# Kernel optimization log

Measured on AMD Instinct MI355X. Metric: run time of the kernel, lower is better.

## Reference

```python
import jax, jax.numpy as jnp
import numpy as np

B, L, D, H = 2, 2048, 1024, 16
HD = D // H


def setup_inputs() -> dict:
    key = jax.random.key(0)
    ks = jax.random.split(key, 14)
    s = 0.02
    return {
        "hidden_states": jax.random.normal(ks[0], (B, L, D), jnp.float32),
        "position_embeddings": jax.random.normal(ks[1], (B, L, D), jnp.float32),
        "Wcq": jax.random.normal(ks[2], (D, D), jnp.float32) * s,
        "bcq": jnp.zeros((D,), jnp.float32),
        "Wck": jax.random.normal(ks[3], (D, D), jnp.float32) * s,
        "bck": jnp.zeros((D,), jnp.float32),
        "Wpq": jax.random.normal(ks[4], (D, D), jnp.float32) * s,
        "bpq": jnp.zeros((D,), jnp.float32),
        "Wpk": jax.random.normal(ks[5], (D, D), jnp.float32) * s,
        "bpk": jnp.zeros((D,), jnp.float32),
        "rel_bias": jnp.zeros((1, H, 1, 1), jnp.float32),
        "Wo": jax.random.normal(ks[6], (D, D), jnp.float32) * s,
        "bo": jnp.zeros((D,), jnp.float32),
    }


def _split_heads(x):
    # [B, L, D] -> [B, H, L, HD]
    b, l, _ = x.shape
    return x.reshape(b, l, H, HD).transpose(0, 2, 1, 3)


def reference(hidden_states, position_embeddings, Wcq, bcq, Wck, bck,
              Wpq, bpq, Wpk, bpk, rel_bias, Wo, bo):
    cq = _split_heads(hidden_states @ Wcq + bcq)
    ck = _split_heads(hidden_states @ Wck + bck)
    # NOTE: original code (faithfully reproduced) uses content_key as the value
    cv = ck
    pq = _split_heads(position_embeddings @ Wpq + bpq)
    pk = _split_heads(position_embeddings @ Wpk + bpk)

    scores = (jnp.einsum("bhqd,bhkd->bhqk", cq, ck)
              + jnp.einsum("bhqd,bhkd->bhqk", pq, pk)
              + rel_bias)
    attn_weights = jax.nn.softmax(scores / jnp.sqrt(jnp.float32(HD)), axis=-1)
    ctx = jnp.einsum("bhqk,bhkd->bhqd", attn_weights, cv)
    ctx = ctx.transpose(0, 2, 1, 3).reshape(hidden_states.shape[0], -1, D)
    output = ctx @ Wo + bo
    return output, attn_weights
```

## Files before the change

kernel.cpp:

```cpp
#include <hip/hip_runtime.h>
#include <hip/hip_bf16.h>
#include <math.h>


#define Bc 2
#define Lc 2048
#define Dc 1024
#define Hc 16
#define Mc (Bc*Lc)
#define NT 32

typedef __attribute__((ext_vector_type(8))) __bf16 bf16x8;
typedef __attribute__((ext_vector_type(4))) float f32x4;
typedef __attribute__((ext_vector_type(16))) float f32x16;
typedef __attribute__((ext_vector_type(2))) unsigned u32x2;

union U4 { unsigned u[4]; bf16x8 v; };

__device__ __forceinline__ void gl_lds16(const void* g, void* l) {
    __builtin_amdgcn_global_load_lds(
        (const __attribute__((address_space(1))) void*)g,
        (__attribute__((address_space(3))) void*)l, 16, 0, 0);
}
__device__ __forceinline__ unsigned pkbf(float a, float b) {
    unsigned short ua = __builtin_bit_cast(unsigned short, (__bf16)a);
    unsigned short ub = __builtin_bit_cast(unsigned short, (__bf16)b);
    return (unsigned)ua | ((unsigned)ub << 16);
}
__device__ __forceinline__ float lo2f(unsigned u){ return __builtin_bit_cast(float, u << 16); }
__device__ __forceinline__ float hi2f(unsigned u){ return __builtin_bit_cast(float, u & 0xffff0000u); }
#define E2(x) __builtin_amdgcn_exp2f(x)

#define WAIT_VM0  asm volatile("s_waitcnt vmcnt(0)" ::: "memory")
#define WAIT_VM2  asm volatile("s_waitcnt vmcnt(2)" ::: "memory")
#define WAIT_VM4  asm volatile("s_waitcnt vmcnt(4)" ::: "memory")
#define WAIT_VM6  asm volatile("s_waitcnt vmcnt(6)" ::: "memory")
#define WAIT_VM8  asm volatile("s_waitcnt vmcnt(8)" ::: "memory")
#define WAIT_VM10 asm volatile("s_waitcnt vmcnt(10)" ::: "memory")
#define WAIT_LG0  asm volatile("s_waitcnt lgkmcnt(0)" ::: "memory")
#define SBAR __builtin_amdgcn_sched_barrier(0)
#define BARRIER do { __builtin_amdgcn_sched_barrier(0); __builtin_amdgcn_s_barrier(); __builtin_amdgcn_sched_barrier(0); } while (0)

__global__ __launch_bounds__(256) void prep_kernel(
    const float* __restrict__ hidden, const float* __restrict__ pos,
    const float* __restrict__ Wcq, const float* __restrict__ Wck,
    const float* __restrict__ Wpq, const float* __restrict__ Wpk,
    const float* __restrict__ Wo,
    __bf16* __restrict__ Wt, __bf16* __restrict__ Woh, __bf16* __restrict__ Wol,
    __bf16* __restrict__ Xh, __bf16* __restrict__ Xp)
{
    const int z = blockIdx.z;
    const int t = threadIdx.x;
    if (z >= 5) {
        const float* X = (z==5) ? hidden : pos;
        __bf16* dst    = (z==5) ? Xh : Xp;
        const size_t base = ((size_t)(blockIdx.y*16 + blockIdx.x)*256 + t) * 128;
        #pragma unroll
        for (int c = 0; c < 16; ++c) {
            const float* sp = X + base + c*8;
            float4 v0 = *(const float4*)sp;
            float4 v1 = *(const float4*)(sp + 4);
            bf16x8 o;
            o[0]=(__bf16)v0.x; o[1]=(__bf16)v0.y; o[2]=(__bf16)v0.z; o[3]=(__bf16)v0.w;
            o[4]=(__bf16)v1.x; o[5]=(__bf16)v1.y; o[6]=(__bf16)v1.z; o[7]=(__bf16)v1.w;
            *(bf16x8*)(dst + base + c*8) = o;
        }
        return;
    }
    const float* W = (z==0)?Wcq:(z==1)?Wck:(z==2)?Wpq:(z==3)?Wpk:Wo;
    const int n  = blockIdx.x*64 + (t & 63);
    const int k0 = blockIdx.y*128 + (t >> 6)*32;
    float v[32];
    #pragma unroll
    for (int j = 0; j < 32; ++j) v[j] = W[(size_t)(k0+j)*Dc + n];
    if (z < 4) {
        __bf16* dst = Wt + (size_t)z*Dc*Dc + (size_t)n*Dc + k0;
        #pragma unroll
        for (int c = 0; c < 4; ++c) {
            bf16x8 o;
            #pragma unroll
            for (int j = 0; j < 8; ++j) o[j] = (__bf16)v[c*8+j];
            *(bf16x8*)(dst + c*8) = o;
        }
    } else {
        __bf16* dh = Woh + (size_t)n*Dc + k0;
        __bf16* dl = Wol + (size_t)n*Dc + k0;
        #pragma unroll
        for (int c = 0; c < 4; ++c) {
            bf16x8 oh, ol;
            #pragma unroll
            for (int j = 0; j < 8; ++j) {
                float x = v[c*8+j];
                __bf16 hi = (__bf16)x;
                oh[j] = hi; ol[j] = (__bf16)(x - (float)hi);
            }
            *(bf16x8*)(dh + c*8) = oh;
            *(bf16x8*)(dl + c*8) = ol;
        }
    }
}

__global__ __launch_bounds__(256) void proj_kernel(
    const __bf16* __restrict__ Xh, const __bf16* __restrict__ Xp,
    const __bf16* __restrict__ Wt,
    const float* __restrict__ bcq, const float* __restrict__ bck,
    const float* __restrict__ bpq, const float* __restrict__ bpk,
    __bf16* __restrict__ Qc, __bf16* __restrict__ Kc)
{
    const int g = blockIdx.x;
    const int nblk = g >> 7, sg = g & 127, mblk = sg & 31, z = sg >> 5;
    const int m0 = mblk*128, n0 = nblk*128;
    const __bf16* X = (z < 2) ? Xh : Xp;
    const __bf16* Wz = Wt + (size_t)z*Dc*Dc;
    const float* bias = (z==0)?bcq:(z==1)?bck:(z==2)?bpq:bpk;
    __bf16* dst = (z & 1) ? Kc : Qc;
    const int half = z >> 1;
    const float scale = (z & 1) ? 1.0f : 0.18033688011112042f;

    const int t = threadIdx.x, lane = t & 63, w = t >> 6;
    const int wm = w >> 1, wn = w & 1;

    __shared__ __align__(16) char smem[49152];

    const int brow4 = lane >> 2;
    const int bcol  = ((lane & 3) ^ (brow4 & 3)) * 8;

    f32x4 acc[4][4] = {};

    #define STAGE_P(B, KT) do { \
        const int k0_ = (KT)*32; \
        _Pragma("unroll") \
        for (int i = 0; i < 2; ++i) { \
            int row = 16*(2*w+i) + brow4; \
            gl_lds16(X  + (size_t)(m0+row)*Dc + k0_ + bcol, smem + (B)*16384 + (2*w+i)*1024); \
            gl_lds16(Wz + (size_t)(n0+row)*Dc + k0_ + bcol, smem + (B)*16384 + 8192 + (2*w+i)*1024); \
        } \
    } while (0)

    STAGE_P(0, 0); STAGE_P(1, 1);
    WAIT_VM4; BARRIER;
    for (int kt = 0; kt < 32; ++kt) {
        if (kt+2 < 32) STAGE_P((kt+2) % 3, kt+2);
        SBAR;
        const int buf = kt % 3;
        bf16x8 a[4], b[4];
        const int s2 = lane >> 4;
        #pragma unroll
        for (int i = 0; i < 4; ++i) {
            int Ra = wm*64 + i*16 + (lane&15);
            int Rb = wn*64 + i*16 + (lane&15);
            a[i] = *(const bf16x8*)(smem + buf*16384 + Ra*64 + ((s2 ^ (Ra&3))*16));
            b[i] = *(const bf16x8*)(smem + buf*16384 + 8192 + Rb*64 + ((s2 ^ (Rb&3))*16));
        }
        __builtin_amdgcn_s_setprio(1);
        #pragma unroll
        for (int mi = 0; mi < 4; ++mi)
            #pragma unroll
            for (int ni = 0; ni < 4; ++ni)
                acc[mi][ni] = __builtin_amdgcn_mfma_f32_16x16x32_bf16(a[mi], b[ni], acc[mi][ni], 0, 0, 0);
        __builtin_amdgcn_s_setprio(0);
        if (kt+2 < 32) { WAIT_VM4; } else { WAIT_VM0; }
        BARRIER;
    }
    #undef STAGE_P
    #pragma unroll
    for (int mi = 0; mi < 4; ++mi)
        #pragma unroll
        for (int ni = 0; ni < 4; ++ni)
            #pragma unroll
            for (int r = 0; r < 4; ++r) {
                int row = m0 + wm*64 + mi*16 + (lane>>4)*4 + r;
                int col = n0 + wn*64 + ni*16 + (lane&15);
                float v = (acc[mi][ni][r] + bias[col]) * scale;
                int bb = row >> 11, l = row & (Lc-1);
                int hh = col >> 6,  hd = col & 63;
                dst[(((size_t)bb*Hc + hh)*Lc + l)*128 + half*64 + hd] = (__bf16)v;
            }
}

__global__ __launch_bounds__(256) void vt_kernel(
    const __bf16* __restrict__ Kc, __bf16* __restrict__ VT)
{
    const int l0 = blockIdx.x * 128, hb = blockIdx.y;
    const int t = threadIdx.x, w = t >> 6, lane = t & 63;
    __shared__ __bf16 T[128][72];
    const __bf16* src = Kc + ((size_t)hb*Lc + l0)*128;
    {
        const int lr = t >> 3, cc = t & 7;
        #pragma unroll
        for (int j = 0; j < 4; ++j)
            *(bf16x8*)&T[lr + j*32][cc*8] = *(const bf16x8*)(src + (size_t)(lr + j*32)*128 + cc*8);
    }
    __syncthreads();
    {
        const int d = lane;
        __bf16* dstp = VT + ((size_t)hb*64 + d)*Lc + l0 + w*32;
        #pragma unroll
        for (int j = 0; j < 4; ++j) {
            bf16x8 o;
            #pragma unroll
            for (int i = 0; i < 8; ++i) o[i] = T[w*32 + j*8 + i][d];
            *(bf16x8*)(dstp + j*8) = o;
        }
    }
}

__global__ __launch_bounds__(512, 4) void attn1_kernel(
    const __bf16* __restrict__ Qc, const __bf16* __restrict__ Kc,
    const float* __restrict__ rel_bias, float* __restrict__ baddp)
{
    const int g = blockIdx.x;
    const int qt = g >> 5, hb = g & 31, h = hb & 15;
    const int q0 = qt * 256;
    const int t = threadIdx.x, lane = t & 63, w = t >> 6;
    const int ln31 = lane & 31, hi = lane >> 5;

    const __bf16* Qp = Qc + (size_t)hb * Lc * 128;
    const __bf16* Kp = Kc + (size_t)hb * Lc * 128;

    __shared__ __align__(16) char smem[49152];

    bf16x8 qa[8];
    {
        const __bf16* qrow = Qp + (size_t)(q0 + w*32 + ln31) * 128 + hi*8;
        #pragma unroll
        for (int ks = 0; ks < 8; ++ks) qa[ks] = *(const bf16x8*)(qrow + ks*16);
    }

    int kof[2];
    #pragma unroll
    for (int c = 0; c < 2; ++c) {
        int rr = w*8 + c*4 + (lane >> 4);
        kof[c] = rr*128 + (((lane & 15) ^ (rr & 15)) * 8);
    }
    int kR[8];
    #pragma unroll
    for (int ks = 0; ks < 8; ++ks) kR[ks] = ((ks*2 + hi) ^ (lane & 15)) * 8;

    #define STAGE_K(B, KT) do { \
        const __bf16* kb_ = Kp + (size_t)(KT)*8192; \
        gl_lds16(kb_ + kof[0], smem + (B)*16384 + (w*8 + 0)*256); \
        gl_lds16(kb_ + kof[1], smem + (B)*16384 + (w*8 + 4)*256); \
    } while (0)
    #define KB(B, ROW, KS) (*(const bf16x8*)(smem + (B)*16384 + (ROW)*256 + kR[KS]*2))

    const float bc = rel_bias[h] * 0.18033688011112042f;
    float lp[4] = {0.f, 0.f, 0.f, 0.f};

    STAGE_K(0, 0); STAGE_K(1, 1);
    WAIT_VM2; BARRIER;
    for (int kt = 0; kt < NT; ++kt) {
        if (kt+2 < NT) STAGE_K((kt+2) % 3, kt+2);
        SBAR;
        const int buf = kt % 3;
        f32x16 s0, s1;
        #pragma unroll
        for (int r = 0; r < 16; ++r) { s0[r] = bc; s1[r] = bc; }
        __builtin_amdgcn_s_setprio(1);
        #pragma unroll
        for (int ks = 0; ks < 8; ++ks) {
            bf16x8 kb0 = KB(buf, ln31, ks);
            bf16x8 kb1 = KB(buf, 32 + ln31, ks);
            s0 = __builtin_amdgcn_mfma_f32_32x32x16_bf16(kb0, qa[ks], s0, 0, 0, 0);
            s1 = __builtin_amdgcn_mfma_f32_32x32x16_bf16(kb1, qa[ks], s1, 0, 0, 0);
        }
        __builtin_amdgcn_s_setprio(0);
        #pragma unroll
        for (int r = 0; r < 16; ++r) {
            lp[r & 3] += E2(s0[r]);
            lp[r & 3] += E2(s1[r]);
        }
        if (kt+2 < NT) { WAIT_VM2; } else { WAIT_VM0; }
        BARRIER;
    }
    float lsum = (lp[0] + lp[1]) + (lp[2] + lp[3]);
    lsum += __shfl_xor(lsum, 32);
    if (!hi) baddp[(size_t)hb*Lc + q0 + w*32 + ln31] = bc - log2f(lsum);
    #undef STAGE_K
    #undef KB
}

__global__ __launch_bounds__(512, 2) void attn2_kernel(
    const __bf16* __restrict__ Qc, const __bf16* __restrict__ Kc,
    const __bf16* __restrict__ VT, const float* __restrict__ baddp,
    float* __restrict__ attn, __bf16* __restrict__ ctxh)
{
    const int g = blockIdx.x;
    const int qt = g >> 5, hb = g & 31, h = hb & 15, bb = hb >> 4;
    const int q0 = qt * 256;
    const int t = threadIdx.x, lane = t & 63, w = t >> 6;
    const int ln31 = lane & 31, hi = lane >> 5;

    const __bf16* Qp = Qc + (size_t)hb * Lc * 128;
    const __bf16* Kp = Kc + (size_t)hb * Lc * 128;
    const __bf16* Vp = VT + (size_t)hb * 64 * Lc;

    __shared__ __align__(16) char smem[98304];
    char* const VsB = smem + 49152;
    char* const PsW = smem + 65536 + w*4096;

    bf16x8 qa[8];
    {
        const __bf16* qrow = Qp + (size_t)(q0 + w*32 + ln31) * 128 + hi*8;
        #pragma unroll
        for (int ks = 0; ks < 8; ++ks) qa[ks] = *(const bf16x8*)(qrow + ks*16);
    }
    const float badd = baddp[(size_t)hb*Lc + q0 + w*32 + ln31];

    int kof[2];
    #pragma unroll
    for (int c = 0; c < 2; ++c) {
        int rr = w*8 + c*4 + (lane >> 4);
        kof[c] = rr*128 + (((lane & 15) ^ (rr & 15)) * 8);
    }
    int vof;
    {
        int dl = lane >> 3;
        int dd = w*8 + dl;
        vof = dd*2048 + (((lane & 7) ^ dl) * 8);
    }
    int kR[8];
    #pragma unroll
    for (int ks = 0; ks < 8; ++ks) kR[ks] = ((ks*2 + hi) ^ (lane & 15)) * 8;
    int vR[4];
    #pragma unroll
    for (int ks = 0; ks < 4; ++ks) vR[ks] = ((ks*2 + hi) ^ (lane & 7)) * 8;

    #define STAGE_K(B, KT) do { \
        const __bf16* kb_ = Kp + (size_t)(KT)*8192; \
        gl_lds16(kb_ + kof[0], smem + (B)*16384 + (w*8 + 0)*256); \
        gl_lds16(kb_ + kof[1], smem + (B)*16384 + (w*8 + 4)*256); \
    } while (0)
    #define STAGE_V(B, KT) do { \
        const __bf16* vb_ = Vp + (KT)*64; \
        gl_lds16(vb_ + vof, VsB + (B)*8192 + (w*8)*128); \
    } while (0)
    #define KB(B, ROW, KS) (*(const bf16x8*)(smem + (B)*16384 + (ROW)*256 + kR[KS]*2))
    #define VB(B, ROW, KS) (*(const bf16x8*)(VsB  + (B)*8192 + (ROW)*128 + vR[KS]*2))

    f32x16 ctx0 = {}, ctx1 = {};
    float* abase = attn + ((size_t)hb*Lc + q0 + w*32)*Lc;
    const int rr2 = lane >> 4;
    const int s8  = lane & 15;

    STAGE_K(0, 0); STAGE_V(0, 0); STAGE_K(1, 1);
    WAIT_VM2; BARRIER;

    for (int kt = 0; kt < NT; ++kt) {
        if (kt+1 < NT) STAGE_V((kt+1) & 1, kt+1);
        if (kt+2 < NT) STAGE_K((kt+2) % 3, kt+2);
        SBAR;
        const int buf = kt % 3;
        f32x16 s0, s1;
        #pragma unroll
        for (int r = 0; r < 16; ++r) { s0[r] = badd; s1[r] = badd; }
        __builtin_amdgcn_s_setprio(1);
        #pragma unroll
        for (int ks = 0; ks < 8; ++ks) {
            bf16x8 kb0 = KB(buf, ln31, ks);
            bf16x8 kb1 = KB(buf, 32 + ln31, ks);
            s0 = __builtin_amdgcn_mfma_f32_32x32x16_bf16(kb0, qa[ks], s0, 0, 0, 0);
            s1 = __builtin_amdgcn_mfma_f32_32x32x16_bf16(kb1, qa[ks], s1, 0, 0, 0);
        }
        __builtin_amdgcn_s_setprio(0);
        unsigned u0[8], u1[8], r0[8], r1[8];
        #pragma unroll
        for (int gq = 0; gq < 4; ++gq) {
            u0[gq]   = pkbf(E2(s0[4*gq+0]), E2(s0[4*gq+1]));
            u1[gq]   = pkbf(E2(s0[4*gq+2]), E2(s0[4*gq+3]));
            u0[4+gq] = pkbf(E2(s1[4*gq+0]), E2(s1[4*gq+1]));
            u1[4+gq] = pkbf(E2(s1[4*gq+2]), E2(s1[4*gq+3]));
        }
        #pragma unroll
        for (int gq = 0; gq < 8; ++gq) {
            r0[gq] = __shfl_xor(u0[gq], 32);
            r1[gq] = __shfl_xor(u1[gq], 32);
        }
        bf16x8 pb[4];
        #pragma unroll
        for (int ks = 0; ks < 4; ++ks) {
            const int gq = 2*ks + hi;
            U4 u;
            u.u[0] = hi ? r0[gq] : u0[gq];
            u.u[1] = hi ? r1[gq] : u1[gq];
            u.u[2] = hi ? u0[gq] : r0[gq];
            u.u[3] = hi ? u1[gq] : r1[gq];
            pb[ks] = u.v;
            *(bf16x8*)(PsW + ln31*128 + ((gq ^ (ln31 & 7))*16)) = u.v;
        }
        __builtin_amdgcn_s_setprio(1);
        #pragma unroll
        for (int ks = 0; ks < 4; ++ks) {
            bf16x8 v0 = VB(kt & 1, ln31, ks);
            bf16x8 v1 = VB(kt & 1, 32 + ln31, ks);
            ctx0 = __builtin_amdgcn_mfma_f32_32x32x16_bf16(pb[ks], v0, ctx0, 0, 0, 0);
            ctx1 = __builtin_amdgcn_mfma_f32_32x32x16_bf16(pb[ks], v1, ctx1, 0, 0, 0);
        }
        __builtin_amdgcn_s_setprio(0);
        WAIT_LG0; SBAR;
        #pragma unroll
        for (int j = 0; j < 8; ++j) {
            const int row = j*4 + rr2;
            u32x2 d = *(const u32x2*)(PsW + row*128 + (((s8>>1) ^ (row&7))*16) + (s8&1)*8);
            f32x4 o;
            o[0]=lo2f(d[0]); o[1]=hi2f(d[0]); o[2]=lo2f(d[1]); o[3]=hi2f(d[1]);
            __builtin_nontemporal_store(o, (f32x4*)(abase + (size_t)row*Lc + kt*64 + s8*4));
        }
        if (kt+1 < NT) {
            if (kt+2 < NT) { WAIT_VM10; } else { WAIT_VM8; }
            BARRIER;
        }
    }

    #pragma unroll
    for (int r = 0; r < 16; ++r) {
        const int R = (r&3) + 8*(r>>2) + 4*hi;
        const size_t row = (size_t)bb*Lc + q0 + w*32 + R;
        ctxh[row*Dc + h*64 + ln31]      = (__bf16)ctx0[r];
        ctxh[row*Dc + h*64 + 32 + ln31] = (__bf16)ctx1[r];
    }
    #undef STAGE_K
    #undef STAGE_V
    #undef KB
    #undef VB
}

__global__ __launch_bounds__(256) void out_kernel(
    const __bf16* __restrict__ ctxh, const __bf16* __restrict__ Woh,
    const __bf16* __restrict__ Wol, const float* __restrict__ bo,
    float* __restrict__ out)
{
    const int m0 = blockIdx.y * 128, n0 = blockIdx.x * 128;
    const int t = threadIdx.x, lane = t & 63, w = t >> 6;
    const int wm = w >> 1, wn = w & 1;

    __shared__ __align__(16) char smem[73728];

    const int row4 = lane >> 2;
    const int scol = ((lane & 3) ^ (row4 & 3)) * 8;

    f32x4 acc[4][4] = {};

    #define STAGE_O(B, KT) do { \
        const int k0_ = (KT)*32; \
        _Pragma("unroll") \
        for (int i = 0; i < 2; ++i) { \
            int row = 16*(2*w+i) + row4; \
            gl_lds16(ctxh + (size_t)(m0+row)*Dc + k0_ + scol, smem + (B)*24576 + (2*w+i)*1024); \
            gl_lds16(Woh  + (size_t)(n0+row)*Dc + k0_ + scol, smem + (B)*24576 + 8192 + (2*w+i)*1024); \
            gl_lds16(Wol  + (size_t)(n0+row)*Dc + k0_ + scol, smem + (B)*24576 + 16384 + (2*w+i)*1024); \
        } \
    } while (0)

    STAGE_O(0, 0); STAGE_O(1, 1);
    WAIT_VM6; BARRIER;
    for (int kt = 0; kt < 32; ++kt) {
        if (kt+2 < 32) STAGE_O((kt+2) % 3, kt+2);
        SBAR;
        const int buf = kt % 3;
        bf16x8 a[4], bh[4], bl[4];
        const int s2 = lane >> 4;
        #pragma unroll
        for (int i = 0; i < 4; ++i) {
            int Ra = wm*64 + i*16 + (lane&15);
            int Rb = wn*64 + i*16 + (lane&15);
            a[i]  = *(const bf16x8*)(smem + buf*24576 + Ra*64 + ((s2 ^ (Ra&3))*16));
            bh[i] = *(const bf16x8*)(smem + buf*24576 + 8192 + Rb*64 + ((s2 ^ (Rb&3))*16));
            bl[i] = *(const bf16x8*)(smem + buf*24576 + 16384 + Rb*64 + ((s2 ^ (Rb&3))*16));
        }
        __builtin_amdgcn_s_setprio(1);
        #pragma unroll
        for (int mi = 0; mi < 4; ++mi)
            #pragma unroll
            for (int ni = 0; ni < 4; ++ni) {
                acc[mi][ni] = __builtin_amdgcn_mfma_f32_16x16x32_bf16(a[mi], bh[ni], acc[mi][ni], 0, 0, 0);
                acc[mi][ni] = __builtin_amdgcn_mfma_f32_16x16x32_bf16(a[mi], bl[ni], acc[mi][ni], 0, 0, 0);
            }
        __builtin_amdgcn_s_setprio(0);
        if (kt+2 < 32) { WAIT_VM6; } else { WAIT_VM0; }
        BARRIER;
    }
    #undef STAGE_O
    #pragma unroll
    for (int mi = 0; mi < 4; ++mi)
        #pragma unroll
        for (int ni = 0; ni < 4; ++ni)
            #pragma unroll
            for (int r = 0; r < 4; ++r) {
                int row = m0 + wm*64 + mi*16 + (lane>>4)*4 + r;
                int col = n0 + wn*64 + ni*16 + (lane&15);
                __builtin_nontemporal_store(acc[mi][ni][r] + bo[col],
                                            out + (size_t)row * Dc + col);
            }
}

extern "C" void kernel_launch(void* const* d_in, const int* in_sizes, int n_in,
                              void* d_out, int out_size, void* d_ws, size_t ws_size,
                              hipStream_t stream)
{
    const float* hidden = (const float*)d_in[0];
    const float* pos    = (const float*)d_in[1];
    const float* Wcq = (const float*)d_in[2];  const float* bcq = (const float*)d_in[3];
    const float* Wck = (const float*)d_in[4];  const float* bck = (const float*)d_in[5];
    const float* Wpq = (const float*)d_in[6];  const float* bpq = (const float*)d_in[7];
    const float* Wpk = (const float*)d_in[8];  const float* bpk = (const float*)d_in[9];
    const float* relb = (const float*)d_in[10];
    const float* Wo  = (const float*)d_in[11]; const float* bo  = (const float*)d_in[12];

    float* out  = (float*)d_out;
    float* attn = out + (size_t)Mc * Dc;

    __bf16* ws   = (__bf16*)d_ws;
    __bf16* Woh  = ws;
    __bf16* Wol  = ws + (1u<<20);
    __bf16* Wt   = ws + (2u<<20);
    __bf16* ctxh = Wt;
    __bf16* Qc   = ws + (6u<<20);
    __bf16* Kc   = ws + (14u<<20);
    __bf16* VTb  = ws + (22u<<20);
    float*  badd = (float*)(ws + (26u<<20));

    __bf16* Xh = (__bf16*)attn;
    __bf16* Xp = Xh + (4u<<20);

    prep_kernel<<<dim3(16, 8, 7), 256, 0, stream>>>(
        hidden, pos, Wcq, Wck, Wpq, Wpk, Wo, Wt, Woh, Wol, Xh, Xp);
    proj_kernel<<<dim3(1024), 256, 0, stream>>>(Xh, Xp, Wt, bcq, bck, bpq, bpk, Qc, Kc);
    vt_kernel<<<dim3(Lc/128, 32), 256, 0, stream>>>(Kc, VTb);
    attn1_kernel<<<dim3(256), 512, 0, stream>>>(Qc, Kc, relb, badd);
    attn2_kernel<<<dim3(256), 512, 0, stream>>>(Qc, Kc, VTb, badd, attn, ctxh);
    out_kernel<<<dim3(8, 32), 256, 0, stream>>>(ctxh, Woh, Wol, bo, out);
}
```

Baseline: 282.3 us.

## Enlarge projection tiles to 256x128 with 512 threads and stage epilogue stores through LDS

The projection GEMM now runs 512-thread blocks, each computing a 256x128 tile. This halves the grid and lets eight waves share each staged weight tile, cutting redundant B loads. Both the projection and output GEMM epilogues now write accumulators to shared memory first, then emit coalesced 16-byte vector stores instead of scattered per-element stores. The cost is larger LDS use (72KB per projection block), which may reduce occupancy, plus an extra block-wide barrier in each epilogue.

```diff
diff --git a/kernel.cpp b/kernel.cpp
--- a/kernel.cpp
+++ b/kernel.cpp
@@ -33,7 +33,7 @@
 
 #define WAIT_VM0  asm volatile("s_waitcnt vmcnt(0)" ::: "memory")
 #define WAIT_VM2  asm volatile("s_waitcnt vmcnt(2)" ::: "memory")
-#define WAIT_VM4  asm volatile("s_waitcnt vmcnt(4)" ::: "memory")
+#define WAIT_VM3  asm volatile("s_waitcnt vmcnt(3)" ::: "memory")
 #define WAIT_VM6  asm volatile("s_waitcnt vmcnt(6)" ::: "memory")
 #define WAIT_VM8  asm volatile("s_waitcnt vmcnt(8)" ::: "memory")
 #define WAIT_VM10 asm volatile("s_waitcnt vmcnt(10)" ::: "memory")
@@ -100,7 +100,7 @@
     }
 }
 
-__global__ __launch_bounds__(256) void proj_kernel(
+__global__ __launch_bounds__(512, 4) void proj_kernel(
     const __bf16* __restrict__ Xh, const __bf16* __restrict__ Xp,
     const __bf16* __restrict__ Wt,
     const float* __restrict__ bcq, const float* __restrict__ bck,
@@ -108,8 +108,8 @@
     __bf16* __restrict__ Qc, __bf16* __restrict__ Kc)
 {
     const int g = blockIdx.x;
-    const int nblk = g >> 7, sg = g & 127, mblk = sg & 31, z = sg >> 5;
-    const int m0 = mblk*128, n0 = nblk*128;
+    const int nblk = g >> 6, z = (g >> 4) & 3, mblk = g & 15;
+    const int m0 = mblk*256, n0 = nblk*128;
     const __bf16* X = (z < 2) ? Xh : Xp;
     const __bf16* Wz = Wt + (size_t)z*Dc*Dc;
     const float* bias = (z==0)?bcq:(z==1)?bck:(z==2)?bpq:bpk;
@@ -120,7 +120,7 @@
     const int t = threadIdx.x, lane = t & 63, w = t >> 6;
     const int wm = w >> 1, wn = w & 1;
 
-    __shared__ __align__(16) char smem[49152];
+    __shared__ __align__(16) char smem[73728];
 
     const int brow4 = lane >> 2;
     const int bcol  = ((lane & 3) ^ (brow4 & 3)) * 8;
@@ -132,13 +132,16 @@
         _Pragma("unroll") \
         for (int i = 0; i < 2; ++i) { \
             int row = 16*(2*w+i) + brow4; \
-            gl_lds16(X  + (size_t)(m0+row)*Dc + k0_ + bcol, smem + (B)*16384 + (2*w+i)*1024); \
-            gl_lds16(Wz + (size_t)(n0+row)*Dc + k0_ + bcol, smem + (B)*16384 + 8192 + (2*w+i)*1024); \
+            gl_lds16(X + (size_t)(m0+row)*Dc + k0_ + bcol, smem + (B)*24576 + (2*w+i)*1024); \
+        } \
+        { \
+            int row = 16*w + brow4; \
+            gl_lds16(Wz + (size_t)(n0+row)*Dc + k0_ + bcol, smem + (B)*24576 + 16384 + w*1024); \
         } \
     } while (0)
 
     STAGE_P(0, 0); STAGE_P(1, 1);
-    WAIT_VM4; BARRIER;
+    WAIT_VM3; BARRIER;
     for (int kt = 0; kt < 32; ++kt) {
         if (kt+2 < 32) STAGE_P((kt+2) % 3, kt+2);
         SBAR;
@@ -149,8 +152,8 @@
         for (int i = 0; i < 4; ++i) {
             int Ra = wm*64 + i*16 + (lane&15);
             int Rb = wn*64 + i*16 + (lane&15);
-            a[i] = *(const bf16x8*)(smem + buf*16384 + Ra*64 + ((s2 ^ (Ra&3))*16));
-            b[i] = *(const bf16x8*)(smem + buf*16384 + 8192 + Rb*64 + ((s2 ^ (Rb&3))*16));
+            a[i] = *(const bf16x8*)(smem + buf*24576 + Ra*64 + ((s2 ^ (Ra&3))*16));
+            b[i] = *(const bf16x8*)(smem + buf*24576 + 16384 + Rb*64 + ((s2 ^ (Rb&3))*16));
         }
         __builtin_amdgcn_s_setprio(1);
         #pragma unroll
@@ -159,23 +162,34 @@
             for (int ni = 0; ni < 4; ++ni)
                 acc[mi][ni] = __builtin_amdgcn_mfma_f32_16x16x32_bf16(a[mi], b[ni], acc[mi][ni], 0, 0, 0);
         __builtin_amdgcn_s_setprio(0);
-        if (kt+2 < 32) { WAIT_VM4; } else { WAIT_VM0; }
+        if (kt+2 < 32) { WAIT_VM3; } else { WAIT_VM0; }
         BARRIER;
     }
     #undef STAGE_P
+
     #pragma unroll
     for (int mi = 0; mi < 4; ++mi)
         #pragma unroll
         for (int ni = 0; ni < 4; ++ni)
             #pragma unroll
             for (int r = 0; r < 4; ++r) {
-                int row = m0 + wm*64 + mi*16 + (lane>>4)*4 + r;
-                int col = n0 + wn*64 + ni*16 + (lane&15);
-                float v = (acc[mi][ni][r] + bias[col]) * scale;
-                int bb = row >> 11, l = row & (Lc-1);
-                int hh = col >> 6,  hd = col & 63;
-                dst[(((size_t)bb*Hc + hh)*Lc + l)*128 + half*64 + hd] = (__bf16)v;
+                int rl = wm*64 + mi*16 + (lane>>4)*4 + r;
+                int cl = wn*64 + ni*16 + (lane&15);
+                float v = (acc[mi][ni][r] + bias[n0 + cl]) * scale;
+                *(__bf16*)(smem + rl*256 + cl*2) = (__bf16)v;
             }
+    __syncthreads();
+    {
+        const int row = t >> 1, seg = t & 1;
+        const int rowg = m0 + row;
+        const int bb = rowg >> 11, l = rowg & (Lc-1);
+        const int hh = (n0 >> 6) + seg;
+        __bf16* dp = dst + (((size_t)bb*Hc + hh)*Lc + l)*128 + half*64;
+        const char* sp = smem + row*256 + seg*128;
+        #pragma unroll
+        for (int j = 0; j < 8; ++j)
+            *(bf16x8*)(dp + j*8) = *(const bf16x8*)(sp + j*16);
+    }
 }
 
 __global__ __launch_bounds__(256) void vt_kernel(
@@ -481,17 +495,26 @@
         BARRIER;
     }
     #undef STAGE_O
+
     #pragma unroll
     for (int mi = 0; mi < 4; ++mi)
         #pragma unroll
         for (int ni = 0; ni < 4; ++ni)
             #pragma unroll
             for (int r = 0; r < 4; ++r) {
-                int row = m0 + wm*64 + mi*16 + (lane>>4)*4 + r;
-                int col = n0 + wn*64 + ni*16 + (lane&15);
-                __builtin_nontemporal_store(acc[mi][ni][r] + bo[col],
-                                            out + (size_t)row * Dc + col);
+                int rl = wm*64 + mi*16 + (lane>>4)*4 + r;
+                int cl = wn*64 + ni*16 + (lane&15);
+                *(float*)(smem + rl*512 + cl*4) = acc[mi][ni][r] + bo[n0 + cl];
             }
+    __syncthreads();
+    {
+        const int row = t >> 1, seg = t & 1;
+        float* dp = out + (size_t)(m0 + row) * Dc + n0 + seg*64;
+        const char* sp = smem + row*512 + seg*256;
+        #pragma unroll
+        for (int j = 0; j < 16; ++j)
+            __builtin_nontemporal_store(*(const f32x4*)(sp + j*16), (f32x4*)(dp + j*4));
+    }
 }
 
 extern "C" void kernel_launch(void* const* d_in, const int* in_sizes, int n_in,
@@ -525,7 +548,7 @@
 
     prep_kernel<<<dim3(16, 8, 7), 256, 0, stream>>>(
         hidden, pos, Wcq, Wck, Wpq, Wpk, Wo, Wt, Woh, Wol, Xh, Xp);
-    proj_kernel<<<dim3(1024), 256, 0, stream>>>(Xh, Xp, Wt, bcq, bck, bpq, bpk, Qc, Kc);
+    proj_kernel<<<dim3(512), 512, 0, stream>>>(Xh, Xp, Wt, bcq, bck, bpq, bpk, Qc, Kc);
     vt_kernel<<<dim3(Lc/128, 32), 256, 0, stream>>>(Kc, VTb);
     attn1_kernel<<<dim3(256), 512, 0, stream>>>(Qc, Kc, relb, badd);
     attn2_kernel<<<dim3(256), 512, 0, stream>>>(Qc, Kc, VTb, badd, attn, ctxh);
```

Result: slower. 318.9 us (+13.0%).
